# Optimization experiments

Hardware: AMD Instinct MI355X
Metric: run time of the kernel (lower is better)

Reference implementation:

```python
import jax, jax.numpy as jnp
import numpy as np

K_MASK = jnp.finfo(jnp.bfloat16).min
ROPE_THETA = 1000000.0


def _rope_sincos(position_ids, head_dim, theta):
    # position_ids: [b, t] int -> sin, cos: [b, t, head_dim//2]
    frac = jnp.arange(0, head_dim, 2, dtype=jnp.float32) / head_dim
    timescale = theta ** frac
    ang = position_ids[..., None].astype(jnp.float32) / timescale
    return jnp.sin(ang), jnp.cos(ang)


def _apply_rope(x, sin, cos):
    # x: [b, t, n, h]; sin/cos: [b, t, h//2]
    h = x.shape[-1]
    x1, x2 = x[..., : h // 2], x[..., h // 2 :]
    s = sin[:, :, None, :]
    c = cos[:, :, None, :]
    return jnp.concatenate([x1 * c - x2 * s, x2 * c + x1 * s], axis=-1).astype(x.dtype)


def setup_inputs() -> dict:
    key = jax.random.key(0)
    ks = jax.random.split(key, 8)
    b, t, S = 8, 16, 8192
    D, N, K, H = 1536, 12, 2, 128
    std = 0.01  # nnx.initializers.normal() default stddev
    return {
        "x": jax.random.normal(ks[0], (b, t, D), jnp.float32),
        "k_cache": jax.random.normal(ks[1], (b, S, K, H), jnp.float32),
        "v_cache": jax.random.normal(ks[2], (b, S, K, H), jnp.float32),
        "wq": jax.random.normal(ks[3], (D, N, H), jnp.float32) * std,
        "bq": jnp.zeros((N, H), jnp.float32),
        "wk": jax.random.normal(ks[4], (D, K, H), jnp.float32) * std,
        "bk": jnp.zeros((K, H), jnp.float32),
        "wv": jax.random.normal(ks[5], (D, K, H), jnp.float32) * std,
        "bv": jnp.zeros((K, H), jnp.float32),
        "wo": jax.random.normal(ks[6], (N, H, D), jnp.float32) * std,
        "segment_ids": jnp.ones((b, t), jnp.int32),
        "start_ind": jnp.zeros((8,), jnp.int32),
        "cur_ind": 4096,
    }


def reference(x, k_cache, v_cache, wq, bq, wk, bk, wv, bv, wo,
              segment_ids, start_ind, cur_ind):
    b, t, D = x.shape
    S = k_cache.shape[1]
    N, H = wq.shape[1], wq.shape[2]
    K = wk.shape[1]
    G = N // K  # n_rep
    scale = H ** -0.5

    # projections with bias
    q = jnp.einsum("btd,dnh->btnh", x, wq) + bq
    kp = jnp.einsum("btd,dkh->btkh", x, wk) + bk
    v = jnp.einsum("btd,dkh->btkh", x, wv) + bv

    # left-pad bookkeeping (count_left_pads) and start index resolution
    nonpad = segment_ids != 0  # [b, t]
    left_pads = jnp.argmax(nonpad, axis=-1).astype(jnp.int32)
    start = jnp.where(start_ind < 0, left_pads, start_ind)  # [b]

    # positions from segment ids, offset by current cache index
    positions = jnp.maximum(jnp.cumsum(nonpad.astype(jnp.int32), axis=-1) - 1, 0) + cur_ind
    sin, cos = _rope_sincos(positions, H, ROPE_THETA)
    q = _apply_rope(q, sin, cos)
    kp = _apply_rope(kp, sin, cos)

    # cache update
    k_cache = jax.lax.dynamic_update_slice(k_cache, kp.astype(k_cache.dtype), (0, cur_ind, 0, 0))
    v_cache = jax.lax.dynamic_update_slice(v_cache, v.astype(v_cache.dtype), (0, cur_ind, 0, 0))

    # GQA attention over full cache
    qg = q.reshape(b, t, K, G, H)
    logits = jnp.einsum("btkgh,bskh->btskg", qg, k_cache) * scale  # [b,t,S,K,G]

    q_pos = cur_ind + jnp.arange(t, dtype=jnp.int32)[None, :] - start[:, None]  # [b,t]
    ts = jnp.arange(S, dtype=jnp.int32)
    kv_seg = (ts[None, :] >= start[:, None]) & (ts[None, :] < cur_ind + t)  # [b,S]
    k_pos = ts[None, :] - start[:, None]
    causal = k_pos[:, None, :] <= q_pos[:, :, None]  # [b,t,S]
    seg = kv_seg[:, None, :].astype(segment_ids.dtype) == segment_ids[:, :, None]  # [b,t,S]
    mask = (causal & seg)[:, :, :, None, None]

    logits = jnp.where(mask, logits, K_MASK)
    w = jax.nn.softmax(logits.astype(jnp.float32), axis=2).astype(logits.dtype)
    qkv = jnp.einsum("btskg,bskh->btkgh", w, v_cache).reshape(b, t, N, H)
    return jnp.einsum("btnh,nhd->btd", qkv, wo)
```

## Files before the change

### kernel.cpp

```cpp
#include <hip/hip_runtime.h>

#define B_ 8
#define T_ 16
#define D_ 1536
#define N_ 12
#define KH_ 2
#define G_ 6
#define H_ 128
#define S_ 8192
#define NCHUNK 16
#define SPLITS 8

typedef __attribute__((ext_vector_type(8))) short bf16x8;
typedef __attribute__((ext_vector_type(4))) float f32x4;
typedef __attribute__((ext_vector_type(4))) unsigned short u16x4;

__device__ __forceinline__ unsigned short f2bf(float x) {
    unsigned u = __float_as_uint(x);
    u += 0x7fffu + ((u >> 16) & 1u);
    return (unsigned short)(u >> 16);
}
__device__ __forceinline__ float bf2f(unsigned short h) {
    return __uint_as_float(((unsigned)h) << 16);
}

__global__ __launch_bounds__(256, 4) void gemm_splitk(
    const float* __restrict__ A,
    const float* __restrict__ W0, int n0, int ldb0,
    const float* __restrict__ W1, int n1, int ldb1,
    const float* __restrict__ W2, int ldb2,
    float* __restrict__ part, int NTOT, int Kdim)
{
    __shared__ __align__(16) unsigned short Ah[64][40], Al[64][40];
    __shared__ __align__(16) unsigned short Bh[64][40], Bl[64][40];
    const int tid = threadIdx.x;
    const int wave = tid >> 6, lane = tid & 63;
    const int col = lane & 15, g = lane >> 4;
    const int row0 = blockIdx.y * 64;
    const int c0 = blockIdx.x * 64;
    const int ks = Kdim / gridDim.z;
    const int k0 = blockIdx.z * ks;

    const float* Bp; int ldb, bc0;
    if (c0 < n0)           { Bp = W0; ldb = ldb0; bc0 = c0; }
    else if (c0 < n0 + n1) { Bp = W1; ldb = ldb1; bc0 = c0 - n0; }
    else                   { Bp = W2; ldb = ldb2; bc0 = c0 - n0 - n1; }

    f32x4 acc[4];
#pragma unroll
    for (int nt = 0; nt < 4; ++nt) acc[nt] = (f32x4){0.f, 0.f, 0.f, 0.f};

    for (int kk = 0; kk < ks; kk += 32) {
        __syncthreads();
        if (tid < 128) {
#pragma unroll
            for (int c = tid; c < 512; c += 128) {
                int r = c >> 3, k4 = c & 7;
                float4 v = *(const float4*)&A[(size_t)(row0 + r) * Kdim + k0 + kk + k4 * 4];
                float f[4] = {v.x, v.y, v.z, v.w};
                u16x4 hv, lv;
#pragma unroll
                for (int i = 0; i < 4; ++i) {
                    unsigned short hh = f2bf(f[i]);
                    hv[i] = hh; lv[i] = f2bf(f[i] - bf2f(hh));
                }
                *(u16x4*)&Ah[r][k4 * 4] = hv;
                *(u16x4*)&Al[r][k4 * 4] = lv;
            }
        } else {
            int t2 = tid - 128;
            int kq = t2 >> 4, cq = t2 & 15;
            float a[4][4];
#pragma unroll
            for (int r = 0; r < 4; ++r) {
                float4 v = *(const float4*)&Bp[(size_t)(k0 + kk + kq * 4 + r) * ldb + bc0 + cq * 4];
                a[r][0] = v.x; a[r][1] = v.y; a[r][2] = v.z; a[r][3] = v.w;
            }
#pragma unroll
            for (int cc = 0; cc < 4; ++cc) {
                u16x4 hv, lv;
#pragma unroll
                for (int r = 0; r < 4; ++r) {
                    unsigned short hh = f2bf(a[r][cc]);
                    hv[r] = hh; lv[r] = f2bf(a[r][cc] - bf2f(hh));
                }
                *(u16x4*)&Bh[cq * 4 + cc][kq * 4] = hv;
                *(u16x4*)&Bl[cq * 4 + cc][kq * 4] = lv;
            }
        }
        __syncthreads();

        bf16x8 ah = *(const bf16x8*)&Ah[wave * 16 + col][g * 8];
        bf16x8 al = *(const bf16x8*)&Al[wave * 16 + col][g * 8];
#pragma unroll
        for (int nt = 0; nt < 4; ++nt) {
            bf16x8 bh = *(const bf16x8*)&Bh[nt * 16 + col][g * 8];
            bf16x8 bl = *(const bf16x8*)&Bl[nt * 16 + col][g * 8];
            acc[nt] = __builtin_amdgcn_mfma_f32_16x16x32_bf16(ah, bh, acc[nt], 0, 0, 0);
            acc[nt] = __builtin_amdgcn_mfma_f32_16x16x32_bf16(ah, bl, acc[nt], 0, 0, 0);
            acc[nt] = __builtin_amdgcn_mfma_f32_16x16x32_bf16(al, bh, acc[nt], 0, 0, 0);
        }
    }
#pragma unroll
    for (int nt = 0; nt < 4; ++nt)
#pragma unroll
        for (int j = 0; j < 4; ++j) {
            size_t prow = (size_t)blockIdx.z * 128 + row0 + wave * 16 + g * 4 + j;
            part[prow * NTOT + c0 + nt * 16 + col] = acc[nt][j];
        }
}

__global__ __launch_bounds__(256) void rope_reduce(
    const float* __restrict__ part,
    const float* __restrict__ bq, const float* __restrict__ bk,
    const float* __restrict__ bv,
    const int* __restrict__ seg, const int* __restrict__ curp,
    float* __restrict__ q_rope, float* __restrict__ k_new,
    float* __restrict__ v_new)
{
    const int row = blockIdx.x;
    const int b = row >> 4, t = row & 15;
    const int tid = threadIdx.x;
    __shared__ float S[2048];
    __shared__ float sc[64][2];

    const int CUR = curp[0];
    int c = 0;
    for (int tt = 0; tt <= t; ++tt) c += (seg[b * T_ + tt] != 0) ? 1 : 0;
    int pos = max(c - 1, 0) + CUR;

    if (tid < 64) {
        float frac = (2.0f * tid) / (float)H_;
        float ts = expf(frac * logf(1000000.0f));
        float ang = (float)pos / ts;
        sc[tid][0] = sinf(ang);
        sc[tid][1] = cosf(ang);
    }
    for (int e = tid; e < 2048; e += 256) {
        float s = 0.f;
#pragma unroll
        for (int sp = 0; sp < SPLITS; ++sp)
            s += part[((size_t)sp * 128 + row) * 2048 + e];
        S[e] = s;
    }
    __syncthreads();

    for (int e = tid; e < 768; e += 256) {
        int n = e >> 6, i = e & 63;
        float x1 = S[n * 128 + i] + bq[n * 128 + i];
        float x2 = S[n * 128 + i + 64] + bq[n * 128 + i + 64];
        float s = sc[i][0], co = sc[i][1];
        q_rope[(size_t)row * 1536 + n * 128 + i]      = x1 * co - x2 * s;
        q_rope[(size_t)row * 1536 + n * 128 + i + 64] = x2 * co + x1 * s;
    }
    if (tid < 128) {
        int n = tid >> 6, i = tid & 63;
        float x1 = S[1536 + n * 128 + i] + bk[n * 128 + i];
        float x2 = S[1536 + n * 128 + i + 64] + bk[n * 128 + i + 64];
        float s = sc[i][0], co = sc[i][1];
        k_new[(size_t)row * 256 + n * 128 + i]      = x1 * co - x2 * s;
        k_new[(size_t)row * 256 + n * 128 + i + 64] = x2 * co + x1 * s;
    }
    v_new[(size_t)row * 256 + tid] = S[1792 + tid] + bv[tid];
}

__global__ __launch_bounds__(384, 2) void attn_mfma(
    const float* __restrict__ q_rope, const float* __restrict__ k_new,
    const float* __restrict__ v_new,
    const float* __restrict__ k_cache, const float* __restrict__ v_cache,
    const int* __restrict__ seg, const int* __restrict__ start_ind,
    const int* __restrict__ curp,
    float* __restrict__ part)
{
    const int chunk = blockIdx.x, b = blockIdx.y, kh = blockIdx.z;
    const int tid = threadIdx.x;
    const int wave = tid >> 6, lane = tid & 63;
    const int col = lane & 15, g = lane >> 4;
    const float scale = 0.088388347648318447f;
    const float NEG_INF = -__builtin_inff();

    const int CUR = curp[0];
    const int SPAN = CUR + T_;
    const int CH = (SPAN + NCHUNK - 1) / NCHUNK;
    const int s0 = chunk * CH;
    const int s1 = min(s0 + CH, SPAN);

    int st = start_ind[b];
    if (st < 0) {
        st = 0;
        for (int tt = 0; tt < T_; ++tt)
            if (seg[b * T_ + tt] != 0) { st = tt; break; }
    }

    __shared__ __align__(16) unsigned short K_hi[32][136], K_lo[32][136];
    __shared__ __align__(16) unsigned short Vt_hi[128][40], Vt_lo[128][40];
    __shared__ __align__(16) unsigned short P_hi[6][16][40], P_lo[6][16][40];

    const int qbase = wave * 16;
    const int qi_a = qbase + col;
    const int t_a = (qi_a * 171) >> 10;
    const int gh_a = qi_a - t_a * G_;
    const float* qp = &q_rope[(((size_t)b * T_ + t_a) * N_ + kh * G_ + gh_a) * H_];
    bf16x8 qh[4], ql[4];
#pragma unroll
    for (int ks = 0; ks < 4; ++ks) {
        float4 va = *(const float4*)&qp[ks * 32 + g * 8];
        float4 vb = *(const float4*)&qp[ks * 32 + g * 8 + 4];
        float f[8] = {va.x, va.y, va.z, va.w, vb.x, vb.y, vb.z, vb.w};
#pragma unroll
        for (int i = 0; i < 8; ++i) {
            float xs = f[i] * scale;
            unsigned short hh = f2bf(xs);
            qh[ks][i] = (short)hh;
            ql[ks][i] = (short)f2bf(xs - bf2f(hh));
        }
    }

    int qpos_r[4], segid_r[4];
#pragma unroll
    for (int j = 0; j < 4; ++j) {
        int qi_c = qbase + g * 4 + j;
        int t_c = (qi_c * 171) >> 10;
        segid_r[j] = seg[b * T_ + t_c];
        qpos_r[j] = CUR + t_c - st;
    }

    float m[4], lsum[4];
#pragma unroll
    for (int j = 0; j < 4; ++j) { m[j] = NEG_INF; lsum[j] = 0.f; }
    f32x4 oacc[8];
#pragma unroll
    for (int nt = 0; nt < 8; ++nt) oacc[nt] = (f32x4){0.f, 0.f, 0.f, 0.f};

    const int vky4 = tid >> 5, vd4 = tid & 31;

    auto issueK = [&](float4* kreg, int stile) {
#pragma unroll
        for (int i = 0; i < 3; ++i) {
            int c = tid + i * 384;
            float4 v = {0.f, 0.f, 0.f, 0.f};
            if (c < 1024) {
                int key = c >> 5, d4 = c & 31;
                int s = stile + key;
                if (s < s1) {
                    const float* src = (s < CUR)
                        ? &k_cache[((((size_t)b * S_ + s) * KH_) + kh) * H_ + d4 * 4]
                        : &k_new[((((size_t)b * T_ + (s - CUR)) * KH_) + kh) * H_ + d4 * 4];
                    v = *(const float4*)src;
                }
            }
            kreg[i] = v;
        }
    };
    auto issueV = [&](float4* vreg, int stile) {
        if (tid < 256) {
#pragma unroll
            for (int r = 0; r < 4; ++r) {
                int s = stile + vky4 * 4 + r;
                float4 v = {0.f, 0.f, 0.f, 0.f};
                if (s < s1) {
                    const float* src = (s < CUR)
                        ? &v_cache[((((size_t)b * S_ + s) * KH_) + kh) * H_ + vd4 * 4]
                        : &v_new[((((size_t)b * T_ + (s - CUR)) * KH_) + kh) * H_ + vd4 * 4];
                    v = *(const float4*)src;
                }
                vreg[r] = v;
            }
        }
    };
    auto convertKV = [&](const float4* kreg, const float4* vreg) {
#pragma unroll
        for (int i = 0; i < 3; ++i) {
            int c = tid + i * 384;
            if (c < 1024) {
                int key = c >> 5, d4 = c & 31;
                float f[4] = {kreg[i].x, kreg[i].y, kreg[i].z, kreg[i].w};
                u16x4 hv, lv;
#pragma unroll
                for (int q = 0; q < 4; ++q) {
                    unsigned short hh = f2bf(f[q]);
                    hv[q] = hh; lv[q] = f2bf(f[q] - bf2f(hh));
                }
                *(u16x4*)&K_hi[key][d4 * 4] = hv;
                *(u16x4*)&K_lo[key][d4 * 4] = lv;
            }
        }
        if (tid < 256) {
            float a[4][4];
#pragma unroll
            for (int r = 0; r < 4; ++r) {
                a[r][0] = vreg[r].x; a[r][1] = vreg[r].y;
                a[r][2] = vreg[r].z; a[r][3] = vreg[r].w;
            }
#pragma unroll
            for (int dd = 0; dd < 4; ++dd) {
                u16x4 hv, lv;
#pragma unroll
                for (int r = 0; r < 4; ++r) {
                    unsigned short hh = f2bf(a[r][dd]);
                    hv[r] = hh; lv[r] = f2bf(a[r][dd] - bf2f(hh));
                }
                *(u16x4*)&Vt_hi[vd4 * 4 + dd][vky4 * 4] = hv;
                *(u16x4*)&Vt_lo[vd4 * 4 + dd][vky4 * 4] = lv;
            }
        }
    };

    auto computeTile = [&](int stile) {
        const bool full = (s1 - stile) > 16;
        f32x4 sacc0 = {0.f, 0.f, 0.f, 0.f}, sacc1 = {0.f, 0.f, 0.f, 0.f};
#pragma unroll
        for (int ks = 0; ks < 4; ++ks) {
            bf16x8 k0h = *(const bf16x8*)&K_hi[col][ks * 32 + g * 8];
            bf16x8 k0l = *(const bf16x8*)&K_lo[col][ks * 32 + g * 8];
            sacc0 = __builtin_amdgcn_mfma_f32_16x16x32_bf16(qh[ks], k0h, sacc0, 0, 0, 0);
            sacc0 = __builtin_amdgcn_mfma_f32_16x16x32_bf16(qh[ks], k0l, sacc0, 0, 0, 0);
            sacc0 = __builtin_amdgcn_mfma_f32_16x16x32_bf16(ql[ks], k0h, sacc0, 0, 0, 0);
        }
        if (full) {
#pragma unroll
            for (int ks = 0; ks < 4; ++ks) {
                bf16x8 k1h = *(const bf16x8*)&K_hi[16 + col][ks * 32 + g * 8];
                bf16x8 k1l = *(const bf16x8*)&K_lo[16 + col][ks * 32 + g * 8];
                sacc1 = __builtin_amdgcn_mfma_f32_16x16x32_bf16(qh[ks], k1h, sacc1, 0, 0, 0);
                sacc1 = __builtin_amdgcn_mfma_f32_16x16x32_bf16(qh[ks], k1l, sacc1, 0, 0, 0);
                sacc1 = __builtin_amdgcn_mfma_f32_16x16x32_bf16(ql[ks], k1h, sacc1, 0, 0, 0);
            }
        }

        float rj[4];
        const int skey0 = stile + col, skey1 = stile + 16 + col;
#pragma unroll
        for (int j = 0; j < 4; ++j) {
            bool v0 = (skey0 < s1) && (skey0 - st <= qpos_r[j]) &&
                      (((skey0 >= st) ? 1 : 0) == segid_r[j]);
            bool v1 = (skey1 < s1) && (skey1 - st <= qpos_r[j]) &&
                      (((skey1 >= st) ? 1 : 0) == segid_r[j]);
            float lg0 = v0 ? sacc0[j] : NEG_INF;
            float lg1 = v1 ? sacc1[j] : NEG_INF;
            float tm = fmaxf(lg0, lg1);
            tm = fmaxf(tm, __shfl_xor(tm, 1));
            tm = fmaxf(tm, __shfl_xor(tm, 2));
            tm = fmaxf(tm, __shfl_xor(tm, 4));
            tm = fmaxf(tm, __shfl_xor(tm, 8));
            float mn = fmaxf(m[j], tm);
            float r, p0, p1;
            if (mn == NEG_INF) { r = 1.f; p0 = 0.f; p1 = 0.f; }
            else {
                r  = __expf(m[j] - mn);
                p0 = __expf(lg0 - mn);
                p1 = __expf(lg1 - mn);
            }
            float ps = p0 + p1;
            ps += __shfl_xor(ps, 1);
            ps += __shfl_xor(ps, 2);
            ps += __shfl_xor(ps, 4);
            ps += __shfl_xor(ps, 8);
            lsum[j] = lsum[j] * r + ps;
            m[j] = mn;
            rj[j] = r;
            int row = g * 4 + j;
            unsigned short h0 = f2bf(p0);
            P_hi[wave][row][col] = h0;
            P_lo[wave][row][col] = f2bf(p0 - bf2f(h0));
            unsigned short h1 = f2bf(p1);
            P_hi[wave][row][16 + col] = h1;
            P_lo[wave][row][16 + col] = f2bf(p1 - bf2f(h1));
        }

#pragma unroll
        for (int nt = 0; nt < 8; ++nt) {
#pragma unroll
            for (int j = 0; j < 4; ++j) oacc[nt][j] *= rj[j];
        }

        bf16x8 pah = *(const bf16x8*)&P_hi[wave][col][g * 8];
        bf16x8 pal = *(const bf16x8*)&P_lo[wave][col][g * 8];
#pragma unroll
        for (int nt = 0; nt < 8; ++nt) {
            bf16x8 vbh = *(const bf16x8*)&Vt_hi[nt * 16 + col][g * 8];
            bf16x8 vbl = *(const bf16x8*)&Vt_lo[nt * 16 + col][g * 8];
            oacc[nt] = __builtin_amdgcn_mfma_f32_16x16x32_bf16(pah, vbh, oacc[nt], 0, 0, 0);
            oacc[nt] = __builtin_amdgcn_mfma_f32_16x16x32_bf16(pah, vbl, oacc[nt], 0, 0, 0);
            oacc[nt] = __builtin_amdgcn_mfma_f32_16x16x32_bf16(pal, vbh, oacc[nt], 0, 0, 0);
        }
    };

    const int ntiles = (s1 - s0 + 31) >> 5;
    float4 kregA[3], vregA[4], kregB[3], vregB[4];

    issueK(kregA, s0); issueV(vregA, s0);
    if (ntiles > 1) { issueK(kregB, s0 + 32); issueV(vregB, s0 + 32); }

    for (int ti = 0; ti < ntiles; ti += 2) {
        {
            convertKV(kregA, vregA);
            __syncthreads();
            if (ti + 2 < ntiles) {
                issueK(kregA, s0 + (ti + 2) * 32);
                issueV(vregA, s0 + (ti + 2) * 32);
            }
            computeTile(s0 + ti * 32);
            __syncthreads();
        }
        if (ti + 1 < ntiles) {
            convertKV(kregB, vregB);
            __syncthreads();
            if (ti + 3 < ntiles) {
                issueK(kregB, s0 + (ti + 3) * 32);
                issueV(vregB, s0 + (ti + 3) * 32);
            }
            computeTile(s0 + (ti + 1) * 32);
            __syncthreads();
        }
    }

    const size_t base_q = (((size_t)chunk * B_ + b) * KH_ + kh) * 96;
#pragma unroll
    for (int j = 0; j < 4; ++j) {
        int qi = qbase + g * 4 + j;
        size_t pb = (base_q + qi) * 132;
        if (col == 0) { part[pb] = m[j]; part[pb + 1] = lsum[j]; }
#pragma unroll
        for (int nt = 0; nt < 8; ++nt)
            part[pb + 2 + nt * 16 + col] = oacc[nt][j];
    }
}

__global__ __launch_bounds__(256) void combine_kernel(
    const float* __restrict__ part, float* __restrict__ qkv)
{
    const int row = blockIdx.x;
    const int b = row >> 4, t = row & 15;
    const int tid = threadIdx.x;
    const int half = tid >> 7, h = tid & 127;
    const size_t cstride = (size_t)B_ * KH_ * 96 * 132;

    for (int nb = 0; nb < N_; nb += 2) {
        int n = nb + half;
        int kh = n / G_, g = n - kh * G_;
        int qi = t * G_ + g;
        size_t base0 = (((size_t)b * KH_ + kh) * 96 + qi) * 132;
        float M = -__builtin_inff();
        for (int c = 0; c < NCHUNK; ++c)
            M = fmaxf(M, part[base0 + c * cstride]);
        float den = 0.f, num = 0.f;
        for (int c = 0; c < NCHUNK; ++c) {
            float mc = part[base0 + c * cstride];
            float e = (M == -__builtin_inff() || mc == -__builtin_inff())
                          ? 0.f : expf(mc - M);
            den += e * part[base0 + c * cstride + 1];
            num += e * part[base0 + c * cstride + 2 + h];
        }
        qkv[(size_t)row * (N_ * H_) + n * H_ + h] = (den > 0.f) ? num / den : 0.f;
    }
}

__global__ __launch_bounds__(256) void sum_reduce(
    const float* __restrict__ part, float* __restrict__ out, int n)
{
    int i = blockIdx.x * 256 + threadIdx.x;
    if (i < n) {
        float s = 0.f;
#pragma unroll
        for (int sp = 0; sp < SPLITS; ++sp) s += part[(size_t)sp * n + i];
        out[i] = s;
    }
}

extern "C" void kernel_launch(void* const* d_in, const int* in_sizes, int n_in,
                              void* d_out, int out_size, void* d_ws, size_t ws_size,
                              hipStream_t stream)
{
    (void)in_sizes; (void)n_in; (void)out_size; (void)ws_size;
    const float* x       = (const float*)d_in[0];
    const float* k_cache = (const float*)d_in[1];
    const float* v_cache = (const float*)d_in[2];
    const float* wq      = (const float*)d_in[3];
    const float* bq      = (const float*)d_in[4];
    const float* wk      = (const float*)d_in[5];
    const float* bk      = (const float*)d_in[6];
    const float* wv      = (const float*)d_in[7];
    const float* bv      = (const float*)d_in[8];
    const float* wo      = (const float*)d_in[9];
    const int*   seg     = (const int*)d_in[10];
    const int*   start_i = (const int*)d_in[11];
    const int*   curp    = (const int*)d_in[12];
    float* out = (float*)d_out;
    float* ws  = (float*)d_ws;

    const size_t PQKV = (size_t)SPLITS * 128 * 2048;
    const size_t QSZ  = (size_t)B_ * T_ * N_ * H_;
    const size_t KSZ  = (size_t)B_ * T_ * KH_ * H_;
    float* partP  = ws;
    float* q_rope = partP + PQKV;
    float* k_new  = q_rope + QSZ;
    float* v_new  = k_new + KSZ;
    float* partA  = v_new + KSZ;
    const size_t PSZ = (size_t)NCHUNK * B_ * KH_ * 96 * 132;
    float* qkv    = partA + PSZ;

    gemm_splitk<<<dim3(32, 2, SPLITS), 256, 0, stream>>>(
        x, wq, 1536, 1536, wk, 256, 256, wv, 256, partP, 2048, D_);

    rope_reduce<<<B_ * T_, 256, 0, stream>>>(partP, bq, bk, bv, seg, curp,
                                             q_rope, k_new, v_new);

    attn_mfma<<<dim3(NCHUNK, B_, KH_), 384, 0, stream>>>(
        q_rope, k_new, v_new, k_cache, v_cache, seg, start_i, curp, partA);

    combine_kernel<<<B_ * T_, 256, 0, stream>>>(partA, qkv);

    gemm_splitk<<<dim3(24, 2, SPLITS), 256, 0, stream>>>(
        qkv, wo, 1536, 1536, wo, 0, 1536, wo, 1536, partP, 1536, N_ * H_);

    sum_reduce<<<(B_ * T_ * D_ + 255) / 256, 256, 0, stream>>>(
        partP, out, B_ * T_ * D_);
}
```

Measured before the change: 95.23 us.

## Drop split-bf16 for PV matmul, double attention chunks, alias workspace buffers

The P·V product now uses a single bf16 MFMA instead of the three-term hi/lo split. That removes the lo conversions, their shared-memory buffers and two thirds of the PV MFMAs, while QK keeps its split precision. The smaller shared-memory footprint allows raising launch bounds to 3 blocks per SM and doubling NCHUNK to 32, which gives more parallelism across the KV sequence. The workspace is rearranged so the QKV partials and the attention partials share memory. The cost is lower precision on the probability and V operands, plus a larger combine step.

```diff
diff --git a/kernel.cpp b/kernel.cpp
--- a/kernel.cpp
+++ b/kernel.cpp
@@ -8,7 +8,7 @@
 #define G_ 6
 #define H_ 128
 #define S_ 8192
-#define NCHUNK 16
+#define NCHUNK 32
 #define SPLITS 8
 
 typedef __attribute__((ext_vector_type(8))) short bf16x8;
@@ -164,7 +164,7 @@
     v_new[(size_t)row * 256 + tid] = S[1792 + tid] + bv[tid];
 }
 
-__global__ __launch_bounds__(384, 2) void attn_mfma(
+__global__ __launch_bounds__(384, 3) void attn_mfma(
     const float* __restrict__ q_rope, const float* __restrict__ k_new,
     const float* __restrict__ v_new,
     const float* __restrict__ k_cache, const float* __restrict__ v_cache,
@@ -193,8 +193,8 @@
     }
 
     __shared__ __align__(16) unsigned short K_hi[32][136], K_lo[32][136];
-    __shared__ __align__(16) unsigned short Vt_hi[128][40], Vt_lo[128][40];
-    __shared__ __align__(16) unsigned short P_hi[6][16][40], P_lo[6][16][40];
+    __shared__ __align__(16) unsigned short Vt_hi[128][40];
+    __shared__ __align__(16) unsigned short P_hi[6][16][40];
 
     const int qbase = wave * 16;
     const int qi_a = qbase + col;
@@ -294,14 +294,10 @@
             }
 #pragma unroll
             for (int dd = 0; dd < 4; ++dd) {
-                u16x4 hv, lv;
-#pragma unroll
-                for (int r = 0; r < 4; ++r) {
-                    unsigned short hh = f2bf(a[r][dd]);
-                    hv[r] = hh; lv[r] = f2bf(a[r][dd] - bf2f(hh));
-                }
+                u16x4 hv;
+#pragma unroll
+                for (int r = 0; r < 4; ++r) hv[r] = f2bf(a[r][dd]);
                 *(u16x4*)&Vt_hi[vd4 * 4 + dd][vky4 * 4] = hv;
-                *(u16x4*)&Vt_lo[vd4 * 4 + dd][vky4 * 4] = lv;
             }
         }
     };
@@ -360,12 +356,8 @@
             m[j] = mn;
             rj[j] = r;
             int row = g * 4 + j;
-            unsigned short h0 = f2bf(p0);
-            P_hi[wave][row][col] = h0;
-            P_lo[wave][row][col] = f2bf(p0 - bf2f(h0));
-            unsigned short h1 = f2bf(p1);
-            P_hi[wave][row][16 + col] = h1;
-            P_lo[wave][row][16 + col] = f2bf(p1 - bf2f(h1));
+            P_hi[wave][row][col]      = f2bf(p0);
+            P_hi[wave][row][16 + col] = f2bf(p1);
         }
 
 #pragma unroll
@@ -375,14 +367,10 @@
         }
 
         bf16x8 pah = *(const bf16x8*)&P_hi[wave][col][g * 8];
-        bf16x8 pal = *(const bf16x8*)&P_lo[wave][col][g * 8];
 #pragma unroll
         for (int nt = 0; nt < 8; ++nt) {
             bf16x8 vbh = *(const bf16x8*)&Vt_hi[nt * 16 + col][g * 8];
-            bf16x8 vbl = *(const bf16x8*)&Vt_lo[nt * 16 + col][g * 8];
             oacc[nt] = __builtin_amdgcn_mfma_f32_16x16x32_bf16(pah, vbh, oacc[nt], 0, 0, 0);
-            oacc[nt] = __builtin_amdgcn_mfma_f32_16x16x32_bf16(pah, vbl, oacc[nt], 0, 0, 0);
-            oacc[nt] = __builtin_amdgcn_mfma_f32_16x16x32_bf16(pal, vbh, oacc[nt], 0, 0, 0);
         }
     };
 
@@ -489,16 +477,15 @@
     float* out = (float*)d_out;
     float* ws  = (float*)d_ws;
 
-    const size_t PQKV = (size_t)SPLITS * 128 * 2048;
+    const size_t PSZ  = (size_t)NCHUNK * B_ * KH_ * 96 * 132;
     const size_t QSZ  = (size_t)B_ * T_ * N_ * H_;
     const size_t KSZ  = (size_t)B_ * T_ * KH_ * H_;
     float* partP  = ws;
-    float* q_rope = partP + PQKV;
+    float* partA  = ws;
+    float* q_rope = ws + PSZ;
     float* k_new  = q_rope + QSZ;
     float* v_new  = k_new + KSZ;
-    float* partA  = v_new + KSZ;
-    const size_t PSZ = (size_t)NCHUNK * B_ * KH_ * 96 * 132;
-    float* qkv    = partA + PSZ;
+    float* qkv    = v_new + KSZ;
 
     gemm_splitk<<<dim3(32, 2, SPLITS), 256, 0, stream>>>(
         x, wq, 1536, 1536, wk, 256, 256, wv, 256, partP, 2048, D_);
```

Measured after the change: 185.1 us. 94.4% more time.
